# Kernel optimization log

Measured on AMD Instinct MI355X. Metric: run time of the kernel, lower is better.

Reference implementation:

```python
import jax, jax.numpy as jnp
import numpy as np

N = 100000
IN_CH = 256
HID = 64
OUT_CH = 40
E1 = 1_600_000
E2 = 3_200_000


def spmm(rows, cols, vals, x, n):
    # out[r] = sum over edges e with rows[e]==r of vals[e] * x[cols[e]]
    return jax.ops.segment_sum(vals[:, None] * x[cols], rows, num_segments=n)


def setup_inputs() -> dict:
    key = jax.random.key(0)
    ks = jax.random.split(key, 12)
    x = jax.random.normal(ks[0], (N, IN_CH), dtype=jnp.float32)
    edge_index = jax.random.randint(ks[1], (2, E1), 0, N, dtype=jnp.int32)
    adj_src = jax.random.randint(ks[2], (E1,), 0, N, dtype=jnp.int32)
    adj_dst = jax.random.randint(ks[3], (E1,), 0, N, dtype=jnp.int32)
    adj_val = jax.random.uniform(ks[4], (E1,), dtype=jnp.float32)
    adj2_src = jax.random.randint(ks[5], (E2,), 0, N, dtype=jnp.int32)
    adj2_dst = jax.random.randint(ks[6], (E2,), 0, N, dtype=jnp.int32)
    adj2_val = jax.random.uniform(ks[7], (E2,), dtype=jnp.float32)
    fc1_w = jax.random.normal(ks[8], (HID, IN_CH), dtype=jnp.float32) * (1.0 / np.sqrt(IN_CH))
    fc_out_w = jax.random.normal(ks[9], (OUT_CH, 3 * HID), dtype=jnp.float32) * (1.0 / np.sqrt(3 * HID))
    fc_out_b = jax.random.normal(ks[10], (OUT_CH,), dtype=jnp.float32) * 0.01
    return {"x": x, "edge_index": edge_index,
            "adj_src": adj_src, "adj_dst": adj_dst, "adj_val": adj_val,
            "adj2_src": adj2_src, "adj2_dst": adj2_dst, "adj2_val": adj2_val,
            "fc1_w": fc1_w, "fc_out_w": fc_out_w, "fc_out_b": fc_out_b}


def reference(x, edge_index, adj_src, adj_dst, adj_val,
              adj2_src, adj2_dst, adj2_val, fc1_w, fc_out_w, fc_out_b):
    # h0 = fc1(x), no bias
    h0 = x @ fc1_w.T                                  # [N, HID]
    # num_layers = 1: one round of 1-hop and 2-hop propagation
    h1 = spmm(adj_src, adj_dst, adj_val, h0, N)       # [N, HID]
    h2 = spmm(adj2_src, adj2_dst, adj2_val, h0, N)    # [N, HID]
    h = jnp.concatenate([h0, h1, h2], axis=1)         # [N, 3*HID]
    # dropout is identity in eval mode
    return h @ fc_out_w.T + fc_out_b                  # [N, OUT_CH]
```

## Files before the change

kernel.cpp:

```cpp
#include <hip/hip_runtime.h>

#define Nn 100000
#define INC 256
#define OC 40
#define GEL 4000000u
#define NB 782
#define CAP 7040
#define CAPH 3744
#define CHUNK 4096
#define OVFCAP 65536
#define BSTRIDE 264

#define MP_OFF   0
#define G_OFF    131072
#define GCUR_OFF 16131072
#define OVFC_OFF (GCUR_OFF + 3128)
#define OVFL_OFF (OVFC_OFF + 8)
#define PAY_OFF  (OVFL_OFF + OVFCAP*12)

typedef __attribute__((ext_vector_type(8))) short bf16x8;
typedef __attribute__((ext_vector_type(4))) float f32x4;

__device__ __forceinline__ unsigned short f2bf(float f) {
    unsigned b = __float_as_uint(f);
    b += 0x7FFFu + ((b >> 16) & 1u);
    return (unsigned short)(b >> 16);
}
__device__ __forceinline__ float bf2f(unsigned short u) {
    return __uint_as_float(((unsigned)u) << 16);
}

__global__ void make_M(const float* __restrict__ fc1_w,
                       const float* __restrict__ fc_out_w,
                       unsigned short* __restrict__ Mb) {
    int j = blockIdx.x;
    int k = threadIdx.x;
    float acc = 0.f;
    if (j < 120) {
        int i = j / 40, o = j - i * 40;
        const float* wrow = fc_out_w + o * 192 + i * 64;
#pragma unroll 8
        for (int t = 0; t < 64; ++t)
            acc = fmaf(wrow[t], fc1_w[t * 256 + k], acc);
    }
    Mb[j * 256 + k] = (j < 120) ? f2bf(acc) : (unsigned short)0;
}

__global__ __launch_bounds__(512, 4) void gemm_mfma(
    const float* __restrict__ x, const unsigned short* __restrict__ Mb,
    const float* __restrict__ bias, float* __restrict__ out,
    unsigned short* __restrict__ g) {
    __shared__ unsigned short mlds[120 * BSTRIDE];
    const int tid = threadIdx.x;
    const int w = tid >> 6;
    const int l = tid & 63;
    const int lane15 = l & 15;
    const int quad = l >> 4;

    for (int i = tid; i < 3840; i += 512) {
        int r = i >> 5;
        int k8 = (i & 31) * 8;
        uint4 v = *(const uint4*)(Mb + r * 256 + k8);
        *(uint4*)(mlds + r * BSTRIDE + k8) = v;
    }
    __syncthreads();

    const int arow = blockIdx.x * 128 + w * 16 + lane15;
    const bool rok = arow < Nn;
    const float* xp = x + (size_t)arow * INC + quad * 8;

    f32x4 acc[8];
#pragma unroll
    for (int c = 0; c < 8; ++c) acc[c] = (f32x4){0.f, 0.f, 0.f, 0.f};

    float4 pa[3], pb_[3];
#pragma unroll
    for (int p = 0; p < 2; ++p) {
        pa[p] = make_float4(0, 0, 0, 0); pb_[p] = make_float4(0, 0, 0, 0);
        if (rok) { pa[p] = *(const float4*)(xp + p * 32); pb_[p] = *(const float4*)(xp + p * 32 + 4); }
    }

#pragma unroll
    for (int kt = 0; kt < 8; ++kt) {
        const int nb = (kt + 2) % 3;
        if (kt + 2 < 8) {
            pa[nb] = make_float4(0, 0, 0, 0); pb_[nb] = make_float4(0, 0, 0, 0);
            if (rok) {
                pa[nb] = *(const float4*)(xp + (kt + 2) * 32);
                pb_[nb] = *(const float4*)(xp + (kt + 2) * 32 + 4);
            }
        }
        const int cu = kt % 3;
        bf16x8 af;
        af[0] = (short)f2bf(pa[cu].x); af[1] = (short)f2bf(pa[cu].y);
        af[2] = (short)f2bf(pa[cu].z); af[3] = (short)f2bf(pa[cu].w);
        af[4] = (short)f2bf(pb_[cu].x); af[5] = (short)f2bf(pb_[cu].y);
        af[6] = (short)f2bf(pb_[cu].z); af[7] = (short)f2bf(pb_[cu].w);
        const unsigned short* bbase = mlds + kt * 32 + quad * 8 + lane15 * BSTRIDE;
#pragma unroll
        for (int ct = 0; ct < 8; ++ct) {
            if (ct * 16 >= 120) break;
            bf16x8 bf = *(const bf16x8*)(bbase + ct * 16 * BSTRIDE);
            acc[ct] = __builtin_amdgcn_mfma_f32_16x16x32_bf16(af, bf, acc[ct], 0, 0, 0);
        }
    }

#pragma unroll
    for (int ct = 0; ct < 8; ++ct) {
        int col = ct * 16 + lane15;
        if (col >= 120) continue;
        int ib = col / 40;
        int cc = col - ib * 40;
        float badd = (ib == 0) ? bias[cc] : 0.f;
#pragma unroll
        for (int reg = 0; reg < 4; ++reg) {
            int gr = blockIdx.x * 128 + w * 16 + quad * 4 + reg;
            if (gr >= Nn) continue;
            float v = acc[ct][reg] + badd;
            if (ib == 0) out[gr * 40 + cc] = v;
            else g[(unsigned)(ib - 1) * GEL + (unsigned)gr * 40u + cc] = f2bf(v);
        }
    }
}

__global__ __launch_bounds__(1024, 8) void partition(
    const int* __restrict__ s1, const int* __restrict__ d1, const float* __restrict__ v1, int E1,
    const int* __restrict__ s2, const int* __restrict__ d2, const float* __restrict__ v2, int E2,
    int* __restrict__ gcur, uint2* __restrict__ payload,
    int* __restrict__ ovf_cnt, unsigned* __restrict__ ovf) {
    __shared__ int cnt[NB];
    __shared__ int loff[NB + 1];
    __shared__ int gbase[NB];
    __shared__ int scanbuf[1024];
    __shared__ uint2 pay[CHUNK];
    __shared__ unsigned short dest16[CHUNK];

    const int t = threadIdx.x;
    const int Etot = E1 + E2;
    const int e0 = blockIdx.x * CHUNK;

    for (int i = t; i < NB; i += 1024) cnt[i] = 0;
    __syncthreads();

    int my_b[4]; int my_rank[4]; unsigned my_p[4]; float my_v[4]; bool my_ok[4];
#pragma unroll
    for (int j = 0; j < 4; ++j) {
        int e = e0 + j * 1024 + t;
        my_ok[j] = (e < Etot);
        if (my_ok[j]) {
            int s, d; float v; unsigned gbit;
            if (e < E1) { s = s1[e]; d = d1[e]; v = v1[e]; gbit = 0u; }
            else { int e2 = e - E1; s = s2[e2]; d = d2[e2]; v = v2[e2]; gbit = 1u; }
            my_b[j] = s >> 7;
            my_p[j] = (unsigned)d | (gbit << 17) | (((unsigned)s & 127u) << 18);
            my_v[j] = v;
            my_rank[j] = atomicAdd(&cnt[my_b[j]], 1);
        }
    }
    __syncthreads();

    int c = (t < NB) ? cnt[t] : 0;
    scanbuf[t] = c;
    __syncthreads();
    for (int off = 1; off < 1024; off <<= 1) {
        int v = (t >= off) ? scanbuf[t - off] : 0;
        __syncthreads();
        scanbuf[t] += v;
        __syncthreads();
    }
    if (t < NB) loff[t] = scanbuf[t] - c;
    if (t == 1023) loff[NB] = scanbuf[1023];
    __syncthreads();

    if (t < NB) {
        int cc = cnt[t];
        gbase[t] = cc ? atomicAdd(&gcur[t], cc) : 0;
    }
    __syncthreads();

#pragma unroll
    for (int j = 0; j < 4; ++j) {
        if (my_ok[j]) {
            int lp = loff[my_b[j]] + my_rank[j];
            pay[lp] = make_uint2(my_p[j], __float_as_uint(my_v[j]));
            dest16[lp] = (unsigned short)my_b[j];
        }
    }
    __syncthreads();

    int tot = loff[NB];
    for (int i = t; i < tot; i += 1024) {
        int b = dest16[i];
        int go = gbase[b] + (i - loff[b]);
        if (go < CAP) payload[(size_t)b * CAP + go] = pay[i];
        else {
            int op = atomicAdd(ovf_cnt, 1);
            if (op < OVFCAP) {
                unsigned px = pay[i].x;
                ovf[3 * op] = ((unsigned)b << 7) | ((px >> 18) & 127u);
                ovf[3 * op + 1] = px;
                ovf[3 * op + 2] = pay[i].y;
            }
        }
    }
}

__global__ __launch_bounds__(640, 7) void bucket_gather(
    const int* __restrict__ gcur, const uint2* __restrict__ payload,
    const unsigned short* __restrict__ g, float* __restrict__ out) {
    __shared__ unsigned spay[CAPH];
    __shared__ int cnt[64];
    __shared__ int rs[65];
    __shared__ int cur[64];
    __shared__ int sb[64];

    const int t = threadIdx.x;
    const int b = blockIdx.x >> 1;
    const unsigned h = blockIdx.x & 1;
    int n = gcur[b];
    n = (n < CAP) ? n : CAP;

    if (t < 64) cnt[t] = 0;
    __syncthreads();

    const uint2* pb = payload + (size_t)b * CAP;
    const unsigned* pbx = (const unsigned*)pb;
    for (int i = t; i < n; i += 640) {
        unsigned r = (pbx[2 * i] >> 18) & 127u;
        if ((r >> 6) == h) atomicAdd(&cnt[r & 63u], 1);
    }
    __syncthreads();

    if (t < 64) sb[t] = cnt[t];
    __syncthreads();
    for (int off = 1; off < 64; off <<= 1) {
        int v = 0;
        if (t < 64 && t >= off) v = sb[t - off];
        __syncthreads();
        if (t < 64) sb[t] += v;
        __syncthreads();
    }
    if (t < 64) { int e = sb[t] - cnt[t]; rs[t] = e; cur[t] = e; }
    if (t == 0) rs[64] = 0;
    __syncthreads();
    if (t == 63) rs[64] = sb[63];
    __syncthreads();

    for (int i = t; i < n; i += 640) {
        uint2 p = pb[i];
        unsigned r = (p.x >> 18) & 127u;
        if ((r >> 6) == h) {
            unsigned q = (unsigned)(__uint_as_float(p.y) * 16383.f + 0.5f);
            int pos = atomicAdd(&cur[r & 63u], 1);
            if (pos < CAPH) spay[pos] = (p.x & 0x3FFFFu) | (q << 18);
            else {
                unsigned s = ((unsigned)b << 7) | r;
                unsigned base = (p.x & 0x1FFFFu) * 40u + ((p.x >> 17) & 1u) * GEL;
                float v = __uint_as_float(p.y);
                for (int cch = 0; cch < 40; ++cch)
                    unsafeAtomicAdd(out + s * 40 + cch, v * bf2f(g[base + cch]));
            }
        }
    }
    __syncthreads();

    const int le = t / 10;
    const int q4 = (t - le * 10) * 4;
    const float VS = 1.0f / 16383.0f;
    int e0 = rs[le], e1 = rs[le + 1];
    e1 = (e1 < CAPH) ? e1 : CAPH;
    float4 a0 = make_float4(0.f, 0.f, 0.f, 0.f);
    float4 a1 = make_float4(0.f, 0.f, 0.f, 0.f);
    int e = e0;
    for (; e + 4 <= e1; e += 4) {
        unsigned p0 = spay[e], p1 = spay[e + 1], p2 = spay[e + 2], p3 = spay[e + 3];
        ushort4 u0 = *(const ushort4*)(g + (p0 & 0x1FFFFu) * 40u + ((p0 >> 17) & 1u) * GEL + q4);
        ushort4 u1 = *(const ushort4*)(g + (p1 & 0x1FFFFu) * 40u + ((p1 >> 17) & 1u) * GEL + q4);
        ushort4 u2 = *(const ushort4*)(g + (p2 & 0x1FFFFu) * 40u + ((p2 >> 17) & 1u) * GEL + q4);
        ushort4 u3 = *(const ushort4*)(g + (p3 & 0x1FFFFu) * 40u + ((p3 >> 17) & 1u) * GEL + q4);
        float v0 = (float)(p0 >> 18) * VS, v1 = (float)(p1 >> 18) * VS;
        float v2 = (float)(p2 >> 18) * VS, v3 = (float)(p3 >> 18) * VS;
        a0.x = fmaf(v0, bf2f(u0.x), a0.x); a0.y = fmaf(v0, bf2f(u0.y), a0.y);
        a0.z = fmaf(v0, bf2f(u0.z), a0.z); a0.w = fmaf(v0, bf2f(u0.w), a0.w);
        a1.x = fmaf(v1, bf2f(u1.x), a1.x); a1.y = fmaf(v1, bf2f(u1.y), a1.y);
        a1.z = fmaf(v1, bf2f(u1.z), a1.z); a1.w = fmaf(v1, bf2f(u1.w), a1.w);
        a0.x = fmaf(v2, bf2f(u2.x), a0.x); a0.y = fmaf(v2, bf2f(u2.y), a0.y);
        a0.z = fmaf(v2, bf2f(u2.z), a0.z); a0.w = fmaf(v2, bf2f(u2.w), a0.w);
        a1.x = fmaf(v3, bf2f(u3.x), a1.x); a1.y = fmaf(v3, bf2f(u3.y), a1.y);
        a1.z = fmaf(v3, bf2f(u3.z), a1.z); a1.w = fmaf(v3, bf2f(u3.w), a1.w);
    }
    for (; e < e1; ++e) {
        unsigned p = spay[e];
        float v = (float)(p >> 18) * VS;
        ushort4 u = *(const ushort4*)(g + (p & 0x1FFFFu) * 40u + ((p >> 17) & 1u) * GEL + q4);
        a0.x = fmaf(v, bf2f(u.x), a0.x); a0.y = fmaf(v, bf2f(u.y), a0.y);
        a0.z = fmaf(v, bf2f(u.z), a0.z); a0.w = fmaf(v, bf2f(u.w), a0.w);
    }
    int gr = b * 128 + h * 64 + le;
    if (gr < Nn && e1 > e0) {
        float* po = out + gr * 40 + q4;
        float4 o = *(float4*)po;
        o.x += a0.x + a1.x; o.y += a0.y + a1.y;
        o.z += a0.z + a1.z; o.w += a0.w + a1.w;
        *(float4*)po = o;
    }
}

__global__ __launch_bounds__(256) void ovf_scatter(
    const int* __restrict__ ovf_cnt, const unsigned* __restrict__ ovf,
    const unsigned short* __restrict__ g, float* __restrict__ out) {
    int n = *ovf_cnt;
    n = (n < OVFCAP) ? n : OVFCAP;
    int total = n * 40;
    for (int i = blockIdx.x * 256 + threadIdx.x; i < total; i += 2048) {
        int idx = i / 40, c = i % 40;
        unsigned s = ovf[3 * idx];
        unsigned p = ovf[3 * idx + 1];
        float v = __uint_as_float(ovf[3 * idx + 2]);
        unsigned dst = p & 0x1FFFFu;
        unsigned gph = (p >> 17) & 1u;
        float gf = bf2f(g[gph * GEL + dst * 40 + c]);
        unsafeAtomicAdd(out + s * 40 + c, v * gf);
    }
}

extern "C" void kernel_launch(void* const* d_in, const int* in_sizes, int n_in,
                              void* d_out, int out_size, void* d_ws, size_t ws_size,
                              hipStream_t stream) {
    const float* x        = (const float*)d_in[0];
    const int*   adj_src  = (const int*)d_in[2];
    const int*   adj_dst  = (const int*)d_in[3];
    const float* adj_val  = (const float*)d_in[4];
    const int*   adj2_src = (const int*)d_in[5];
    const int*   adj2_dst = (const int*)d_in[6];
    const float* adj2_val = (const float*)d_in[7];
    const float* fc1_w    = (const float*)d_in[8];
    const float* fc_out_w = (const float*)d_in[9];
    const float* fc_out_b = (const float*)d_in[10];
    float* out = (float*)d_out;

    char* ws = (char*)d_ws;
    unsigned short* Mb      = (unsigned short*)(ws + MP_OFF);
    unsigned short* g       = (unsigned short*)(ws + G_OFF);
    int*            gcur    = (int*)(ws + GCUR_OFF);
    int*            ovf_cnt = (int*)(ws + OVFC_OFF);
    unsigned*       ovf     = (unsigned*)(ws + OVFL_OFF);
    uint2*          payload = (uint2*)(ws + PAY_OFF);

    const int E1 = in_sizes[2];
    const int E2 = in_sizes[5];
    const int Etot = E1 + E2;

    make_M<<<128, 256, 0, stream>>>(fc1_w, fc_out_w, Mb);
    gemm_mfma<<<(Nn + 127) / 128, 512, 0, stream>>>(x, Mb, fc_out_b, out, g);

    hipMemsetAsync(gcur, 0, NB * sizeof(int) + 16, stream);
    partition<<<(Etot + CHUNK - 1) / CHUNK, 1024, 0, stream>>>(
        adj_src, adj_dst, adj_val, E1, adj2_src, adj2_dst, adj2_val, E2,
        gcur, payload, ovf_cnt, ovf);
    bucket_gather<<<NB * 2, 640, 0, stream>>>(gcur, payload, g, out);
    ovf_scatter<<<8, 256, 0, stream>>>(ovf_cnt, ovf, g, out);
}
```

Measured before the change: 394.4 us.

## Use 64-row buckets, register-cached payload sort, and 16-byte gathers with split reduction

```diff
diff --git a/kernel.cpp b/kernel.cpp
--- a/kernel.cpp
+++ b/kernel.cpp
@@ -3,18 +3,17 @@
 #define Nn 100000
 #define INC 256
 #define OC 40
-#define GEL 4000000u
-#define NB 782
-#define CAP 7040
-#define CAPH 3744
+#define GEL 5242880u
+#define NB 1563
+#define CAP64 3744
 #define CHUNK 4096
 #define OVFCAP 65536
 #define BSTRIDE 264
 
 #define MP_OFF   0
 #define G_OFF    131072
-#define GCUR_OFF 16131072
-#define OVFC_OFF (GCUR_OFF + 3128)
+#define GCUR_OFF (G_OFF + 20971520)
+#define OVFC_OFF (GCUR_OFF + 6256)
 #define OVFL_OFF (OVFC_OFF + 8)
 #define PAY_OFF  (OVFL_OFF + OVFCAP*12)
 
@@ -28,6 +27,17 @@
 }
 __device__ __forceinline__ float bf2f(unsigned short u) {
     return __uint_as_float(((unsigned)u) << 16);
+}
+
+__device__ __forceinline__ void fma8(float4& a0, float4& a1, uint4 u, float v) {
+    a0.x = fmaf(v, __uint_as_float(u.x << 16), a0.x);
+    a0.y = fmaf(v, __uint_as_float(u.x & 0xFFFF0000u), a0.y);
+    a0.z = fmaf(v, __uint_as_float(u.y << 16), a0.z);
+    a0.w = fmaf(v, __uint_as_float(u.y & 0xFFFF0000u), a0.w);
+    a1.x = fmaf(v, __uint_as_float(u.z << 16), a1.x);
+    a1.y = fmaf(v, __uint_as_float(u.z & 0xFFFF0000u), a1.y);
+    a1.z = fmaf(v, __uint_as_float(u.w << 16), a1.z);
+    a1.w = fmaf(v, __uint_as_float(u.w & 0xFFFF0000u), a1.w);
 }
 
 __global__ void make_M(const float* __restrict__ fc1_w,
@@ -151,16 +161,17 @@
             int s, d; float v; unsigned gbit;
             if (e < E1) { s = s1[e]; d = d1[e]; v = v1[e]; gbit = 0u; }
             else { int e2 = e - E1; s = s2[e2]; d = d2[e2]; v = v2[e2]; gbit = 1u; }
-            my_b[j] = s >> 7;
-            my_p[j] = (unsigned)d | (gbit << 17) | (((unsigned)s & 127u) << 18);
+            my_b[j] = s >> 6;
+            my_p[j] = (unsigned)d | (gbit << 17) | (((unsigned)s & 63u) << 18);
             my_v[j] = v;
             my_rank[j] = atomicAdd(&cnt[my_b[j]], 1);
         }
     }
     __syncthreads();
 
-    int c = (t < NB) ? cnt[t] : 0;
-    scanbuf[t] = c;
+    int c0 = (2 * t < NB) ? cnt[2 * t] : 0;
+    int c1 = (2 * t + 1 < NB) ? cnt[2 * t + 1] : 0;
+    scanbuf[t] = c0 + c1;
     __syncthreads();
     for (int off = 1; off < 1024; off <<= 1) {
         int v = (t >= off) ? scanbuf[t - off] : 0;
@@ -168,13 +179,15 @@
         scanbuf[t] += v;
         __syncthreads();
     }
-    if (t < NB) loff[t] = scanbuf[t] - c;
-    if (t == 1023) loff[NB] = scanbuf[1023];
-    __syncthreads();
-
-    if (t < NB) {
-        int cc = cnt[t];
-        gbase[t] = cc ? atomicAdd(&gcur[t], cc) : 0;
+    int ex = scanbuf[t] - (c0 + c1);
+    if (2 * t < NB)     loff[2 * t] = ex;
+    if (2 * t + 1 < NB) loff[2 * t + 1] = ex + c0;
+    if (t == 1023)      loff[NB] = scanbuf[1023];
+    __syncthreads();
+
+    for (int i = t; i < NB; i += 1024) {
+        int cc = cnt[i];
+        gbase[i] = cc ? atomicAdd(&gcur[i], cc) : 0;
     }
     __syncthreads();
 
@@ -192,12 +205,12 @@
     for (int i = t; i < tot; i += 1024) {
         int b = dest16[i];
         int go = gbase[b] + (i - loff[b]);
-        if (go < CAP) payload[(size_t)b * CAP + go] = pay[i];
+        if (go < CAP64) payload[(size_t)b * CAP64 + go] = pay[i];
         else {
             int op = atomicAdd(ovf_cnt, 1);
             if (op < OVFCAP) {
                 unsigned px = pay[i].x;
-                ovf[3 * op] = ((unsigned)b << 7) | ((px >> 18) & 127u);
+                ovf[3 * op] = ((unsigned)b << 6) | ((px >> 18) & 63u);
                 ovf[3 * op + 1] = px;
                 ovf[3 * op + 2] = pay[i].y;
             }
@@ -208,26 +221,31 @@
 __global__ __launch_bounds__(640, 7) void bucket_gather(
     const int* __restrict__ gcur, const uint2* __restrict__ payload,
     const unsigned short* __restrict__ g, float* __restrict__ out) {
-    __shared__ unsigned spay[CAPH];
+    __shared__ unsigned spay[CAP64];
     __shared__ int cnt[64];
+    __shared__ int sb[64];
     __shared__ int rs[65];
-    __shared__ int cur[64];
-    __shared__ int sb[64];
+    __shared__ float4 red4[64][10];
 
     const int t = threadIdx.x;
-    const int b = blockIdx.x >> 1;
-    const unsigned h = blockIdx.x & 1;
+    const int b = blockIdx.x;
     int n = gcur[b];
-    n = (n < CAP) ? n : CAP;
+    n = (n < CAP64) ? n : CAP64;
 
     if (t < 64) cnt[t] = 0;
     __syncthreads();
 
-    const uint2* pb = payload + (size_t)b * CAP;
-    const unsigned* pbx = (const unsigned*)pb;
-    for (int i = t; i < n; i += 640) {
-        unsigned r = (pbx[2 * i] >> 18) & 127u;
-        if ((r >> 6) == h) atomicAdd(&cnt[r & 63u], 1);
+    const uint2* pb = payload + (size_t)b * CAP64;
+
+    uint2 pe[6]; int rk[6];
+#pragma unroll
+    for (int j = 0; j < 6; ++j) {
+        int i = t + j * 640;
+        if (i < n) {
+            uint2 p = pb[i];
+            pe[j] = p;
+            rk[j] = atomicAdd(&cnt[(p.x >> 18) & 63u], 1);
+        }
     }
     __syncthreads();
 
@@ -240,69 +258,71 @@
         if (t < 64) sb[t] += v;
         __syncthreads();
     }
-    if (t < 64) { int e = sb[t] - cnt[t]; rs[t] = e; cur[t] = e; }
-    if (t == 0) rs[64] = 0;
-    __syncthreads();
+    if (t < 64) rs[t] = sb[t] - cnt[t];
     if (t == 63) rs[64] = sb[63];
     __syncthreads();
 
-    for (int i = t; i < n; i += 640) {
-        uint2 p = pb[i];
-        unsigned r = (p.x >> 18) & 127u;
-        if ((r >> 6) == h) {
+#pragma unroll
+    for (int j = 0; j < 6; ++j) {
+        int i = t + j * 640;
+        if (i < n) {
+            uint2 p = pe[j];
+            int pos = rs[(p.x >> 18) & 63u] + rk[j];
             unsigned q = (unsigned)(__uint_as_float(p.y) * 16383.f + 0.5f);
-            int pos = atomicAdd(&cur[r & 63u], 1);
-            if (pos < CAPH) spay[pos] = (p.x & 0x3FFFFu) | (q << 18);
-            else {
-                unsigned s = ((unsigned)b << 7) | r;
-                unsigned base = (p.x & 0x1FFFFu) * 40u + ((p.x >> 17) & 1u) * GEL;
-                float v = __uint_as_float(p.y);
-                for (int cch = 0; cch < 40; ++cch)
-                    unsafeAtomicAdd(out + s * 40 + cch, v * bf2f(g[base + cch]));
-            }
+            spay[pos] = (p.x & 0x3FFFFu) | (q << 18);
         }
     }
     __syncthreads();
 
     const int le = t / 10;
-    const int q4 = (t - le * 10) * 4;
+    const int sub = t - le * 10;
+    const int grp = (sub >= 5) ? 1 : 0;
+    const int q8 = (sub - grp * 5) * 8;
     const float VS = 1.0f / 16383.0f;
-    int e0 = rs[le], e1 = rs[le + 1];
-    e1 = (e1 < CAPH) ? e1 : CAPH;
+
     float4 a0 = make_float4(0.f, 0.f, 0.f, 0.f);
-    float4 a1 = make_float4(0.f, 0.f, 0.f, 0.f);
-    int e = e0;
-    for (; e + 4 <= e1; e += 4) {
-        unsigned p0 = spay[e], p1 = spay[e + 1], p2 = spay[e + 2], p3 = spay[e + 3];
-        ushort4 u0 = *(const ushort4*)(g + (p0 & 0x1FFFFu) * 40u + ((p0 >> 17) & 1u) * GEL + q4);
-        ushort4 u1 = *(const ushort4*)(g + (p1 & 0x1FFFFu) * 40u + ((p1 >> 17) & 1u) * GEL + q4);
-        ushort4 u2 = *(const ushort4*)(g + (p2 & 0x1FFFFu) * 40u + ((p2 >> 17) & 1u) * GEL + q4);
-        ushort4 u3 = *(const ushort4*)(g + (p3 & 0x1FFFFu) * 40u + ((p3 >> 17) & 1u) * GEL + q4);
-        float v0 = (float)(p0 >> 18) * VS, v1 = (float)(p1 >> 18) * VS;
-        float v2 = (float)(p2 >> 18) * VS, v3 = (float)(p3 >> 18) * VS;
-        a0.x = fmaf(v0, bf2f(u0.x), a0.x); a0.y = fmaf(v0, bf2f(u0.y), a0.y);
-        a0.z = fmaf(v0, bf2f(u0.z), a0.z); a0.w = fmaf(v0, bf2f(u0.w), a0.w);
-        a1.x = fmaf(v1, bf2f(u1.x), a1.x); a1.y = fmaf(v1, bf2f(u1.y), a1.y);
-        a1.z = fmaf(v1, bf2f(u1.z), a1.z); a1.w = fmaf(v1, bf2f(u1.w), a1.w);
-        a0.x = fmaf(v2, bf2f(u2.x), a0.x); a0.y = fmaf(v2, bf2f(u2.y), a0.y);
-        a0.z = fmaf(v2, bf2f(u2.z), a0.z); a0.w = fmaf(v2, bf2f(u2.w), a0.w);
-        a1.x = fmaf(v3, bf2f(u3.x), a1.x); a1.y = fmaf(v3, bf2f(u3.y), a1.y);
-        a1.z = fmaf(v3, bf2f(u3.z), a1.z); a1.w = fmaf(v3, bf2f(u3.w), a1.w);
-    }
-    for (; e < e1; ++e) {
+    float4 a1 = a0, b0 = a0, b1 = a0;
+    const int estart = rs[le];
+    const int eend = rs[le + 1];
+    int e = estart + grp;
+    for (; e + 6 < eend; e += 8) {
+        unsigned p0 = spay[e], p1 = spay[e + 2], p2 = spay[e + 4], p3 = spay[e + 6];
+        uint4 u0 = *(const uint4*)(g + (p0 & 0x3FFFFu) * 40u + q8);
+        uint4 u1 = *(const uint4*)(g + (p1 & 0x3FFFFu) * 40u + q8);
+        uint4 u2 = *(const uint4*)(g + (p2 & 0x3FFFFu) * 40u + q8);
+        uint4 u3 = *(const uint4*)(g + (p3 & 0x3FFFFu) * 40u + q8);
+        fma8(a0, a1, u0, (float)(p0 >> 18) * VS);
+        fma8(b0, b1, u1, (float)(p1 >> 18) * VS);
+        fma8(a0, a1, u2, (float)(p2 >> 18) * VS);
+        fma8(b0, b1, u3, (float)(p3 >> 18) * VS);
+    }
+    for (; e < eend; e += 2) {
         unsigned p = spay[e];
-        float v = (float)(p >> 18) * VS;
-        ushort4 u = *(const ushort4*)(g + (p & 0x1FFFFu) * 40u + ((p >> 17) & 1u) * GEL + q4);
-        a0.x = fmaf(v, bf2f(u.x), a0.x); a0.y = fmaf(v, bf2f(u.y), a0.y);
-        a0.z = fmaf(v, bf2f(u.z), a0.z); a0.w = fmaf(v, bf2f(u.w), a0.w);
-    }
-    int gr = b * 128 + h * 64 + le;
-    if (gr < Nn && e1 > e0) {
-        float* po = out + gr * 40 + q4;
-        float4 o = *(float4*)po;
-        o.x += a0.x + a1.x; o.y += a0.y + a1.y;
-        o.z += a0.z + a1.z; o.w += a0.w + a1.w;
-        *(float4*)po = o;
+        uint4 u = *(const uint4*)(g + (p & 0x3FFFFu) * 40u + q8);
+        fma8(a0, a1, u, (float)(p >> 18) * VS);
+    }
+    a0.x += b0.x; a0.y += b0.y; a0.z += b0.z; a0.w += b0.w;
+    a1.x += b1.x; a1.y += b1.y; a1.z += b1.z; a1.w += b1.w;
+
+    const int c2 = (q8 >> 2);
+    __syncthreads();
+    if (grp == 1) { red4[le][c2] = a0; red4[le][c2 + 1] = a1; }
+    __syncthreads();
+    if (grp == 0) {
+        float4 r0 = red4[le][c2];
+        float4 r1 = red4[le][c2 + 1];
+        int gr = b * 64 + le;
+        if (gr < Nn && eend > estart) {
+            float* po = out + gr * 40 + q8;
+            float4 o0 = *(const float4*)po;
+            o0.x += a0.x + r0.x; o0.y += a0.y + r0.y;
+            o0.z += a0.z + r0.z; o0.w += a0.w + r0.w;
+            *(float4*)po = o0;
+            float4 o1 = *(const float4*)(po + 4);
+            o1.x += a1.x + r1.x; o1.y += a1.y + r1.y;
+            o1.z += a1.z + r1.z; o1.w += a1.w + r1.w;
+            *(float4*)(po + 4) = o1;
+        }
     }
 }
 
@@ -317,9 +337,8 @@
         unsigned s = ovf[3 * idx];
         unsigned p = ovf[3 * idx + 1];
         float v = __uint_as_float(ovf[3 * idx + 2]);
-        unsigned dst = p & 0x1FFFFu;
-        unsigned gph = (p >> 17) & 1u;
-        float gf = bf2f(g[gph * GEL + dst * 40 + c]);
+        unsigned rid = p & 0x3FFFFu;
+        float gf = bf2f(g[rid * 40u + c]);
         unsafeAtomicAdd(out + s * 40 + c, v * gf);
     }
 }
@@ -354,10 +373,10 @@
     make_M<<<128, 256, 0, stream>>>(fc1_w, fc_out_w, Mb);
     gemm_mfma<<<(Nn + 127) / 128, 512, 0, stream>>>(x, Mb, fc_out_b, out, g);
 
-    hipMemsetAsync(gcur, 0, NB * sizeof(int) + 16, stream);
+    hipMemsetAsync(gcur, 0, (OVFC_OFF - GCUR_OFF) + 8, stream);
     partition<<<(Etot + CHUNK - 1) / CHUNK, 1024, 0, stream>>>(
         adj_src, adj_dst, adj_val, E1, adj2_src, adj2_dst, adj2_val, E2,
         gcur, payload, ovf_cnt, ovf);
-    bucket_gather<<<NB * 2, 640, 0, stream>>>(gcur, payload, g, out);
+    bucket_gather<<<NB, 640, 0, stream>>>(gcur, payload, g, out);
     ovf_scatter<<<8, 256, 0, stream>>>(ovf_cnt, ovf, g, out);
 }
```

New measurement: 384.5 us. 2.5% less time.

## Replace per-row CSR sort in bucket gather with LDS atomic accumulation

Applied to the files above, without the earlier changes.

```diff
diff --git a/kernel.cpp b/kernel.cpp
--- a/kernel.cpp
+++ b/kernel.cpp
@@ -3,19 +3,19 @@
 #define Nn 100000
 #define INC 256
 #define OC 40
-#define GEL 4000000u
+#define GEL 5242880u
 #define NB 782
 #define CAP 7040
-#define CAPH 3744
 #define CHUNK 4096
 #define OVFCAP 65536
 #define BSTRIDE 264
+#define APITCH 41
 
 #define MP_OFF   0
 #define G_OFF    131072
-#define GCUR_OFF 16131072
-#define OVFC_OFF (GCUR_OFF + 3128)
-#define OVFL_OFF (OVFC_OFF + 8)
+#define GCUR_OFF (G_OFF + 20971520)
+#define OVFC_OFF (GCUR_OFF + 3200)
+#define OVFL_OFF (OVFC_OFF + 16)
 #define PAY_OFF  (OVFL_OFF + OVFCAP*12)
 
 typedef __attribute__((ext_vector_type(8))) short bf16x8;
@@ -205,104 +205,66 @@
     }
 }
 
-__global__ __launch_bounds__(640, 7) void bucket_gather(
+__global__ __launch_bounds__(640, 8) void bucket_gather(
     const int* __restrict__ gcur, const uint2* __restrict__ payload,
     const unsigned short* __restrict__ g, float* __restrict__ out) {
-    __shared__ unsigned spay[CAPH];
-    __shared__ int cnt[64];
-    __shared__ int rs[65];
-    __shared__ int cur[64];
-    __shared__ int sb[64];
+    __shared__ float accum[128 * APITCH];
 
     const int t = threadIdx.x;
-    const int b = blockIdx.x >> 1;
-    const unsigned h = blockIdx.x & 1;
+    const int b = blockIdx.x;
+
+    for (int i = t; i < 128 * APITCH; i += 640) accum[i] = 0.f;
     int n = gcur[b];
     n = (n < CAP) ? n : CAP;
-
-    if (t < 64) cnt[t] = 0;
     __syncthreads();
 
     const uint2* pb = payload + (size_t)b * CAP;
-    const unsigned* pbx = (const unsigned*)pb;
-    for (int i = t; i < n; i += 640) {
-        unsigned r = (pbx[2 * i] >> 18) & 127u;
-        if ((r >> 6) == h) atomicAdd(&cnt[r & 63u], 1);
-    }
-    __syncthreads();
-
-    if (t < 64) sb[t] = cnt[t];
-    __syncthreads();
-    for (int off = 1; off < 64; off <<= 1) {
-        int v = 0;
-        if (t < 64 && t >= off) v = sb[t - off];
-        __syncthreads();
-        if (t < 64) sb[t] += v;
-        __syncthreads();
-    }
-    if (t < 64) { int e = sb[t] - cnt[t]; rs[t] = e; cur[t] = e; }
-    if (t == 0) rs[64] = 0;
-    __syncthreads();
-    if (t == 63) rs[64] = sb[63];
-    __syncthreads();
-
-    for (int i = t; i < n; i += 640) {
-        uint2 p = pb[i];
-        unsigned r = (p.x >> 18) & 127u;
-        if ((r >> 6) == h) {
-            unsigned q = (unsigned)(__uint_as_float(p.y) * 16383.f + 0.5f);
-            int pos = atomicAdd(&cur[r & 63u], 1);
-            if (pos < CAPH) spay[pos] = (p.x & 0x3FFFFu) | (q << 18);
-            else {
-                unsigned s = ((unsigned)b << 7) | r;
-                unsigned base = (p.x & 0x1FFFFu) * 40u + ((p.x >> 17) & 1u) * GEL;
-                float v = __uint_as_float(p.y);
-                for (int cch = 0; cch < 40; ++cch)
-                    unsafeAtomicAdd(out + s * 40 + cch, v * bf2f(g[base + cch]));
-            }
-        }
-    }
-    __syncthreads();
-
-    const int le = t / 10;
-    const int q4 = (t - le * 10) * 4;
-    const float VS = 1.0f / 16383.0f;
-    int e0 = rs[le], e1 = rs[le + 1];
-    e1 = (e1 < CAPH) ? e1 : CAPH;
-    float4 a0 = make_float4(0.f, 0.f, 0.f, 0.f);
-    float4 a1 = make_float4(0.f, 0.f, 0.f, 0.f);
-    int e = e0;
-    for (; e + 4 <= e1; e += 4) {
-        unsigned p0 = spay[e], p1 = spay[e + 1], p2 = spay[e + 2], p3 = spay[e + 3];
-        ushort4 u0 = *(const ushort4*)(g + (p0 & 0x1FFFFu) * 40u + ((p0 >> 17) & 1u) * GEL + q4);
-        ushort4 u1 = *(const ushort4*)(g + (p1 & 0x1FFFFu) * 40u + ((p1 >> 17) & 1u) * GEL + q4);
-        ushort4 u2 = *(const ushort4*)(g + (p2 & 0x1FFFFu) * 40u + ((p2 >> 17) & 1u) * GEL + q4);
-        ushort4 u3 = *(const ushort4*)(g + (p3 & 0x1FFFFu) * 40u + ((p3 >> 17) & 1u) * GEL + q4);
-        float v0 = (float)(p0 >> 18) * VS, v1 = (float)(p1 >> 18) * VS;
-        float v2 = (float)(p2 >> 18) * VS, v3 = (float)(p3 >> 18) * VS;
-        a0.x = fmaf(v0, bf2f(u0.x), a0.x); a0.y = fmaf(v0, bf2f(u0.y), a0.y);
-        a0.z = fmaf(v0, bf2f(u0.z), a0.z); a0.w = fmaf(v0, bf2f(u0.w), a0.w);
-        a1.x = fmaf(v1, bf2f(u1.x), a1.x); a1.y = fmaf(v1, bf2f(u1.y), a1.y);
-        a1.z = fmaf(v1, bf2f(u1.z), a1.z); a1.w = fmaf(v1, bf2f(u1.w), a1.w);
-        a0.x = fmaf(v2, bf2f(u2.x), a0.x); a0.y = fmaf(v2, bf2f(u2.y), a0.y);
-        a0.z = fmaf(v2, bf2f(u2.z), a0.z); a0.w = fmaf(v2, bf2f(u2.w), a0.w);
-        a1.x = fmaf(v3, bf2f(u3.x), a1.x); a1.y = fmaf(v3, bf2f(u3.y), a1.y);
-        a1.z = fmaf(v3, bf2f(u3.z), a1.z); a1.w = fmaf(v3, bf2f(u3.w), a1.w);
-    }
-    for (; e < e1; ++e) {
-        unsigned p = spay[e];
-        float v = (float)(p >> 18) * VS;
-        ushort4 u = *(const ushort4*)(g + (p & 0x1FFFFu) * 40u + ((p >> 17) & 1u) * GEL + q4);
-        a0.x = fmaf(v, bf2f(u.x), a0.x); a0.y = fmaf(v, bf2f(u.y), a0.y);
-        a0.z = fmaf(v, bf2f(u.z), a0.z); a0.w = fmaf(v, bf2f(u.w), a0.w);
-    }
-    int gr = b * 128 + h * 64 + le;
-    if (gr < Nn && e1 > e0) {
-        float* po = out + gr * 40 + q4;
-        float4 o = *(float4*)po;
-        o.x += a0.x + a1.x; o.y += a0.y + a1.y;
-        o.z += a0.z + a1.z; o.w += a0.w + a1.w;
-        *(float4*)po = o;
+    const int grp = t / 5;
+    const int q8 = (t - grp * 5) * 8;
+
+    int i = grp;
+    uint2 pc; uint4 uc;
+    if (i < n) {
+        pc = pb[i];
+        uc = *(const uint4*)(g + (pc.x & 0x3FFFFu) * 40u + q8);
+    }
+    while (i < n) {
+        int j = i + 128;
+        uint2 pn; uint4 un;
+        if (j < n) {
+            pn = pb[j];
+            un = *(const uint4*)(g + (pn.x & 0x3FFFFu) * 40u + q8);
+        }
+        {
+            float v = __uint_as_float(pc.y);
+            int row = (pc.x >> 18) & 127;
+            float* ap = accum + row * APITCH + q8;
+            atomicAdd(ap + 0, v * __uint_as_float(uc.x << 16));
+            atomicAdd(ap + 1, v * __uint_as_float(uc.x & 0xFFFF0000u));
+            atomicAdd(ap + 2, v * __uint_as_float(uc.y << 16));
+            atomicAdd(ap + 3, v * __uint_as_float(uc.y & 0xFFFF0000u));
+            atomicAdd(ap + 4, v * __uint_as_float(uc.z << 16));
+            atomicAdd(ap + 5, v * __uint_as_float(uc.z & 0xFFFF0000u));
+            atomicAdd(ap + 6, v * __uint_as_float(uc.w << 16));
+            atomicAdd(ap + 7, v * __uint_as_float(uc.w & 0xFFFF0000u));
+        }
+        pc = pn; uc = un; i = j;
+    }
+    __syncthreads();
+
+    const int row = grp;
+    const int gr = b * 128 + row;
+    if (gr < Nn) {
+        const float* ap = accum + row * APITCH + q8;
+        float s0 = ap[0], s1 = ap[1], s2 = ap[2], s3 = ap[3];
+        float s4 = ap[4], s5 = ap[5], s6 = ap[6], s7 = ap[7];
+        float* po = out + gr * 40 + q8;
+        float4 o0 = *(const float4*)po;
+        o0.x += s0; o0.y += s1; o0.z += s2; o0.w += s3;
+        *(float4*)po = o0;
+        float4 o1 = *(const float4*)(po + 4);
+        o1.x += s4; o1.y += s5; o1.z += s6; o1.w += s7;
+        *(float4*)(po + 4) = o1;
     }
 }
 
@@ -317,9 +279,8 @@
         unsigned s = ovf[3 * idx];
         unsigned p = ovf[3 * idx + 1];
         float v = __uint_as_float(ovf[3 * idx + 2]);
-        unsigned dst = p & 0x1FFFFu;
-        unsigned gph = (p >> 17) & 1u;
-        float gf = bf2f(g[gph * GEL + dst * 40 + c]);
+        unsigned rid = p & 0x3FFFFu;
+        float gf = bf2f(g[rid * 40u + c]);
         unsafeAtomicAdd(out + s * 40 + c, v * gf);
     }
 }
@@ -354,10 +315,10 @@
     make_M<<<128, 256, 0, stream>>>(fc1_w, fc_out_w, Mb);
     gemm_mfma<<<(Nn + 127) / 128, 512, 0, stream>>>(x, Mb, fc_out_b, out, g);
 
-    hipMemsetAsync(gcur, 0, NB * sizeof(int) + 16, stream);
+    hipMemsetAsync(gcur, 0, (OVFC_OFF - GCUR_OFF) + 16, stream);
     partition<<<(Etot + CHUNK - 1) / CHUNK, 1024, 0, stream>>>(
         adj_src, adj_dst, adj_val, E1, adj2_src, adj2_dst, adj2_val, E2,
         gcur, payload, ovf_cnt, ovf);
-    bucket_gather<<<NB * 2, 640, 0, stream>>>(gcur, payload, g, out);
+    bucket_gather<<<NB, 640, 0, stream>>>(gcur, payload, g, out);
     ovf_scatter<<<8, 256, 0, stream>>>(ovf_cnt, ovf, g, out);
 }
```

Result: slower. 1.526 ms (+286.9%).
